# Kernel tuning notes

Hardware: AMD Instinct MI355X
Metric: run time of the kernel (lower is better)

Reference implementation:

```python
import jax, jax.numpy as jnp
import numpy as np

B = 4096          # batch_size * world_size
D = 256           # embedding dim
TEMP = 0.5        # temperature
EPS = 1e-8


def setup_inputs() -> dict:
    key = jax.random.key(0)
    k1, k2 = jax.random.split(key)
    z_i = jax.random.normal(k1, (B, D), dtype=jnp.float32)
    z_j = jax.random.normal(k2, (B, D), dtype=jnp.float32)
    return {"z_i": z_i, "z_j": z_j}


def reference(z_i, z_j):
    N = 2 * B
    z = jnp.concatenate([z_i, z_j], axis=0)                      # [N, D]
    # cosine similarity = normalized dot products (normalize + GEMM)
    norm = jnp.sqrt(jnp.sum(z * z, axis=-1, keepdims=True))
    zn = z / jnp.maximum(norm, EPS)
    sim = (zn @ zn.T) / TEMP                                     # [N, N]
    # positives: pairs (i, i+B) and (i+B, i)
    idx = jnp.arange(N)
    pos = sim[idx, (idx + B) % N]                                # [N]
    # CE with label 0 over [pos, negatives]; the candidate set equals the
    # full sim row minus the diagonal (pos is re-included), so:
    sim_masked = jnp.where(jnp.eye(N, dtype=bool), -jnp.inf, sim)
    lse = jax.nn.logsumexp(sim_masked, axis=1)                   # [N]
    loss = jnp.sum(lse - pos) / N                                # reduction='sum' then /N
    return loss
```

## Files before the change

### kernel.cpp

```cpp
#include <hip/hip_runtime.h>
#include <hip/hip_bf16.h>
#include <cmath>

#define B_SZ 4096
#define N_SZ 8192
#define D_SZ 256
#define EPS 1e-8f
#define EXPC 0.01127105500694503f
#define EXPB -2.8853900817779268f

typedef __attribute__((ext_vector_type(4))) float f32x4;
typedef __attribute__((ext_vector_type(4))) int   i32x4;
typedef __attribute__((ext_vector_type(8))) int   i32x8;


__global__ __launch_bounds__(256) void prep_kernel(const float* __restrict__ zi,
                                                   const float* __restrict__ zj,
                                                   char* __restrict__ znb,
                                                   float* __restrict__ pos) {
    const int wave = threadIdx.x >> 6, lane = threadIdx.x & 63;
    const int i = blockIdx.x * 4 + wave;
    float4 a = reinterpret_cast<const float4*>(zi + (size_t)i * D_SZ)[lane];
    float4 b = reinterpret_cast<const float4*>(zj + (size_t)i * D_SZ)[lane];
    float ssa = a.x * a.x + a.y * a.y + a.z * a.z + a.w * a.w;
    float ssb = b.x * b.x + b.y * b.y + b.z * b.z + b.w * b.w;
    float dab = a.x * b.x + a.y * b.y + a.z * b.z + a.w * b.w;
    #pragma unroll
    for (int off = 32; off; off >>= 1) {
        ssa += __shfl_xor(ssa, off, 64);
        ssb += __shfl_xor(ssb, off, 64);
        dab += __shfl_xor(dab, off, 64);
    }
    const float invna = 1.0f / fmaxf(sqrtf(ssa), EPS);
    const float invnb = 1.0f / fmaxf(sqrtf(ssb), EPS);
    if (lane == 0) {
        float p = dab * invna * invnb * 2.0f;
        pos[i] = p;
        pos[i + B_SZ] = p;
    }
    const float sa = invna * 16.0f, sb = invnb * 16.0f;
    const int koff = (lane >> 2) * 1024 + (lane & 3) * 4;
    {
        int pk = __builtin_amdgcn_cvt_pk_fp8_f32(a.x * sa, a.y * sa, 0, false);
        pk     = __builtin_amdgcn_cvt_pk_fp8_f32(a.z * sa, a.w * sa, pk, true);
        *reinterpret_cast<int*>(znb + (size_t)(i >> 6) * 16384 + koff + (i & 63) * 16) = pk;
    }
    {
        const int r = i + B_SZ;
        int pk = __builtin_amdgcn_cvt_pk_fp8_f32(b.x * sb, b.y * sb, 0, false);
        pk     = __builtin_amdgcn_cvt_pk_fp8_f32(b.z * sb, b.w * sb, pk, true);
        *reinterpret_cast<int*>(znb + (size_t)(r >> 6) * 16384 + koff + (r & 63) * 16) = pk;
    }
}

__global__ __launch_bounds__(256, 2) void simlse_kernel(const char* __restrict__ znb,
                                                        float* __restrict__ partial) {
    const int t = threadIdx.x;
    const int wave = t >> 6, lane = t & 63;

    int bid = blockIdx.x, rt = 0;
    #pragma unroll 1
    for (; rt < 32; ++rt) {
        int cnt = 32 - rt;
        if (bid < cnt) break;
        bid -= cnt;
    }
    const int chunk = rt + bid;
    const bool offdiag = (rt != chunk);
    __shared__ float cs[4][256];

    const int rl = lane & 15;
    const int kg = lane >> 4;
    const int i0 = rt * 256 + wave * 64;

    const char* ap = znb + (size_t)(rt * 4 + wave) * 16384 + rl * 16;
    i32x8 afrag[4][2];
    #pragma unroll
    for (int g = 0; g < 4; ++g)
        #pragma unroll
        for (int kc = 0; kc < 2; ++kc) {
            i32x4 lo = *reinterpret_cast<const i32x4*>(
                ap + (kc * 8 + kg * 2) * 1024 + g * 256);
            i32x4 hi = *reinterpret_cast<const i32x4*>(
                ap + (kc * 8 + kg * 2 + 1) * 1024 + g * 256);
            afrag[g][kc] = __builtin_shufflevector(lo, hi, 0, 1, 2, 3, 4, 5, 6, 7);
        }

    float s_acc[4][4];
    #pragma unroll
    for (int g = 0; g < 4; ++g)
        #pragma unroll
        for (int r = 0; r < 4; ++r) s_acc[g][r] = 0.0f;

    const char* bp0 = znb + (size_t)chunk * 4 * 16384 + kg * 2048 + rl * 16;

    i32x4 nb0 = *reinterpret_cast<const i32x4*>(bp0);
    i32x4 nb1 = *reinterpret_cast<const i32x4*>(bp0 + 1024);
    i32x4 nb2 = *reinterpret_cast<const i32x4*>(bp0 + 8192);
    i32x4 nb3 = *reinterpret_cast<const i32x4*>(bp0 + 9216);

    i32x8 bf0, bf1;
    f32x4 accA[4], accB[4];

    #define PREP_B(F)                                                             \
        {                                                                         \
            bf0 = __builtin_shufflevector(nb0, nb1, 0, 1, 2, 3, 4, 5, 6, 7);      \
            bf1 = __builtin_shufflevector(nb2, nb3, 0, 1, 2, 3, 4, 5, 6, 7);      \
            if ((F) < 15) {                                                       \
                const char* bq = bp0 + (((F) + 1) >> 2) * 16384 +                 \
                                 (((F) + 1) & 3) * 256;                           \
                nb0 = *reinterpret_cast<const i32x4*>(bq);                        \
                nb1 = *reinterpret_cast<const i32x4*>(bq + 1024);                 \
                nb2 = *reinterpret_cast<const i32x4*>(bq + 8192);                 \
                nb3 = *reinterpret_cast<const i32x4*>(bq + 9216);                 \
            }                                                                     \
        }

    #define MFMA8(ACC)                                                            \
        {                                                                         \
            _Pragma("unroll")                                                     \
            for (int g = 0; g < 4; ++g) ACC[g] = (f32x4){0.f, 0.f, 0.f, 0.f};     \
            _Pragma("unroll")                                                     \
            for (int g = 0; g < 4; ++g)                                           \
                asm("v_mfma_f32_16x16x128_f8f6f4 %0, %1, %2, %0"                  \
                    : "+v"(ACC[g]) : "v"(afrag[g][0]), "v"(bf0));                 \
            _Pragma("unroll")                                                     \
            for (int g = 0; g < 4; ++g)                                           \
                asm("v_mfma_f32_16x16x128_f8f6f4 %0, %1, %2, %0"                  \
                    : "+v"(ACC[g]) : "v"(afrag[g][1]), "v"(bf1));                 \
        }

    #define EXPSUM(ACC, F)                                                        \
        {                                                                         \
            float cthr = 0.0f;                                                    \
            _Pragma("unroll")                                                     \
            for (int g = 0; g < 4; ++g)                                           \
                _Pragma("unroll")                                                 \
                for (int r = 0; r < 4; ++r) {                                     \
                    float e = __builtin_amdgcn_exp2f(fmaf(ACC[g][r], EXPC, EXPB)); \
                    s_acc[g][r] += e;                                             \
                    cthr += e;                                                    \
                }                                                                 \
            cthr += __shfl_xor(cthr, 16, 64);                                     \
            cthr += __shfl_xor(cthr, 32, 64);                                     \
            if (offdiag && lane < 16)                                             \
                cs[wave][((F) >> 2) * 64 + ((F) & 3) * 16 + rl] = cthr;           \
        }

    PREP_B(0);
    MFMA8(accA);
    #pragma unroll 1
    for (int fo = 0; fo < 7; ++fo) {
        const int f1 = 2 * fo + 1, f2 = 2 * fo + 2;
        PREP_B(f1); MFMA8(accB);
        asm volatile("s_nop 7");
        EXPSUM(accA, f1 - 1);
        PREP_B(f2); MFMA8(accA);
        asm volatile("s_nop 7");
        EXPSUM(accB, f2 - 1);
    }
    PREP_B(15); MFMA8(accB);
    asm volatile("s_nop 7");
    EXPSUM(accA, 14);
    asm volatile("s_nop 7");
    EXPSUM(accB, 15);

    #pragma unroll
    for (int g = 0; g < 4; ++g)
        #pragma unroll
        for (int r = 0; r < 4; ++r) {
            float v = s_acc[g][r];
            #pragma unroll
            for (int off = 1; off < 16; off <<= 1) v += __shfl_xor(v, off, 64);
            if (rl == 0)
                partial[chunk * N_SZ + i0 + g * 16 + kg * 4 + r] = v;
        }

    if (offdiag) {
        __syncthreads();
        float v = cs[0][t] + cs[1][t] + cs[2][t] + cs[3][t];
        partial[rt * N_SZ + chunk * 256 + t] = v;
    }
    #undef PREP_B
    #undef MFMA8
    #undef EXPSUM
}

__global__ __launch_bounds__(256) void rowsum_kernel(const float* __restrict__ partial,
                                                     const float* __restrict__ pos,
                                                     float* __restrict__ bpart) {
    const int row = blockIdx.x * 256 + threadIdx.x;
    float s = -1.0f;
    #pragma unroll
    for (int c = 0; c < 32; ++c) s += partial[c * N_SZ + row];
    float acc = 2.0f + logf(s) - pos[row];
    #pragma unroll
    for (int off = 32; off; off >>= 1) acc += __shfl_xor(acc, off, 64);
    __shared__ float w[4];
    if ((threadIdx.x & 63) == 0) w[threadIdx.x >> 6] = acc;
    __syncthreads();
    if (threadIdx.x == 0) bpart[blockIdx.x] = w[0] + w[1] + w[2] + w[3];
}

__global__ __launch_bounds__(64) void finsum_kernel(const float* __restrict__ bpart,
                                                    float* __restrict__ out) {
    float v = threadIdx.x < 32 ? bpart[threadIdx.x] : 0.0f;
    #pragma unroll
    for (int off = 32; off; off >>= 1) v += __shfl_xor(v, off, 64);
    if (threadIdx.x == 0) out[0] = v / (float)N_SZ;
}

extern "C" void kernel_launch(void* const* d_in, const int* in_sizes, int n_in,
                              void* d_out, int out_size, void* d_ws, size_t ws_size,
                              hipStream_t stream) {
    const float* zi = (const float*)d_in[0];
    const float* zj = (const float*)d_in[1];

    char* ws = (char*)d_ws;
    char* znb      = ws;
    float* pos     = (float*)(ws + 2097152);
    float* partial = (float*)(ws + 2097152 + 32768);
    float* bpart   = (float*)(ws + 2097152 + 32768 + 1048576);
    float* out = (float*)d_out;

    prep_kernel<<<B_SZ / 4, 256, 0, stream>>>(zi, zj, znb, pos);
    simlse_kernel<<<528, 256, 0, stream>>>(znb, partial);
    rowsum_kernel<<<32, 256, 0, stream>>>(partial, pos, bpart);
    finsum_kernel<<<1, 64, 0, stream>>>(bpart, out);
}
```

Before: 35.12 us.

## Split sim tile columns into 128-wide halves to double block count

Each block of the triangular similarity/LSE kernel now covers a 256-row by 128-column tile instead of 256x256, so the grid grows from 528 to 1056 blocks. Row and column partial sums go to two separate buffers, and rowsum_kernel walks a variable-length range per row tile. The aim is better wave balance and occupancy across the CUs. The cost is more per-block overhead, since A fragments are reloaded twice as often, and a more irregular reduction.

```diff
diff --git a/kernel.cpp b/kernel.cpp
--- a/kernel.cpp
+++ b/kernel.cpp
@@ -54,20 +54,21 @@
 }
 
 __global__ __launch_bounds__(256, 2) void simlse_kernel(const char* __restrict__ znb,
-                                                        float* __restrict__ partial) {
+                                                        float* __restrict__ partial1,
+                                                        float* __restrict__ partial2) {
     const int t = threadIdx.x;
     const int wave = t >> 6, lane = t & 63;
 
     int bid = blockIdx.x, rt = 0;
     #pragma unroll 1
     for (; rt < 32; ++rt) {
-        int cnt = 32 - rt;
+        int cnt = 64 - 2 * rt;
         if (bid < cnt) break;
         bid -= cnt;
     }
-    const int chunk = rt + bid;
-    const bool offdiag = (rt != chunk);
-    __shared__ float cs[4][256];
+    const int c2 = 2 * rt + bid;
+    const bool offdiag = ((c2 >> 1) != rt);
+    __shared__ float cs[4][128];
 
     const int rl = lane & 15;
     const int kg = lane >> 4;
@@ -92,28 +93,28 @@
         #pragma unroll
         for (int r = 0; r < 4; ++r) s_acc[g][r] = 0.0f;
 
-    const char* bp0 = znb + (size_t)chunk * 4 * 16384 + kg * 2048 + rl * 16;
-
-    i32x4 nb0 = *reinterpret_cast<const i32x4*>(bp0);
-    i32x4 nb1 = *reinterpret_cast<const i32x4*>(bp0 + 1024);
-    i32x4 nb2 = *reinterpret_cast<const i32x4*>(bp0 + 8192);
-    i32x4 nb3 = *reinterpret_cast<const i32x4*>(bp0 + 9216);
-
+    const char* bp0 = znb + (size_t)c2 * 2 * 16384 + kg * 2048 + rl * 16;
+
+    i32x4 nbA0, nbA1, nbA2, nbA3;
+    i32x4 nbB0, nbB1, nbB2, nbB3;
     i32x8 bf0, bf1;
     f32x4 accA[4], accB[4];
 
-    #define PREP_B(F)                                                             \
-        {                                                                         \
-            bf0 = __builtin_shufflevector(nb0, nb1, 0, 1, 2, 3, 4, 5, 6, 7);      \
-            bf1 = __builtin_shufflevector(nb2, nb3, 0, 1, 2, 3, 4, 5, 6, 7);      \
-            if ((F) < 15) {                                                       \
-                const char* bq = bp0 + (((F) + 1) >> 2) * 16384 +                 \
-                                 (((F) + 1) & 3) * 256;                           \
-                nb0 = *reinterpret_cast<const i32x4*>(bq);                        \
-                nb1 = *reinterpret_cast<const i32x4*>(bq + 1024);                 \
-                nb2 = *reinterpret_cast<const i32x4*>(bq + 8192);                 \
-                nb3 = *reinterpret_cast<const i32x4*>(bq + 9216);                 \
-            }                                                                     \
+    #define LOAD_A(F)                                                             \
+        {                                                                         \
+            const char* bq = bp0 + ((F) >> 2) * 16384 + ((F) & 3) * 256;          \
+            nbA0 = *reinterpret_cast<const i32x4*>(bq);                           \
+            nbA1 = *reinterpret_cast<const i32x4*>(bq + 1024);                    \
+            nbA2 = *reinterpret_cast<const i32x4*>(bq + 8192);                    \
+            nbA3 = *reinterpret_cast<const i32x4*>(bq + 9216);                    \
+        }
+    #define LOAD_B(F)                                                             \
+        {                                                                         \
+            const char* bq = bp0 + ((F) >> 2) * 16384 + ((F) & 3) * 256;          \
+            nbB0 = *reinterpret_cast<const i32x4*>(bq);                           \
+            nbB1 = *reinterpret_cast<const i32x4*>(bq + 1024);                    \
+            nbB2 = *reinterpret_cast<const i32x4*>(bq + 8192);                    \
+            nbB3 = *reinterpret_cast<const i32x4*>(bq + 9216);                    \
         }
 
     #define MFMA8(ACC)                                                            \
@@ -147,23 +148,35 @@
                 cs[wave][((F) >> 2) * 64 + ((F) & 3) * 16 + rl] = cthr;           \
         }
 
-    PREP_B(0);
+    LOAD_A(0);
+    LOAD_B(1);
+    bf0 = __builtin_shufflevector(nbA0, nbA1, 0, 1, 2, 3, 4, 5, 6, 7);
+    bf1 = __builtin_shufflevector(nbA2, nbA3, 0, 1, 2, 3, 4, 5, 6, 7);
+    LOAD_A(2);
     MFMA8(accA);
     #pragma unroll 1
-    for (int fo = 0; fo < 7; ++fo) {
+    for (int fo = 0; fo < 3; ++fo) {
         const int f1 = 2 * fo + 1, f2 = 2 * fo + 2;
-        PREP_B(f1); MFMA8(accB);
+        bf0 = __builtin_shufflevector(nbB0, nbB1, 0, 1, 2, 3, 4, 5, 6, 7);
+        bf1 = __builtin_shufflevector(nbB2, nbB3, 0, 1, 2, 3, 4, 5, 6, 7);
+        if (f1 + 2 < 8) LOAD_B(f1 + 2);
+        MFMA8(accB);
         asm volatile("s_nop 7");
         EXPSUM(accA, f1 - 1);
-        PREP_B(f2); MFMA8(accA);
+        bf0 = __builtin_shufflevector(nbA0, nbA1, 0, 1, 2, 3, 4, 5, 6, 7);
+        bf1 = __builtin_shufflevector(nbA2, nbA3, 0, 1, 2, 3, 4, 5, 6, 7);
+        if (f2 + 2 < 8) LOAD_A(f2 + 2);
+        MFMA8(accA);
         asm volatile("s_nop 7");
         EXPSUM(accB, f2 - 1);
     }
-    PREP_B(15); MFMA8(accB);
+    bf0 = __builtin_shufflevector(nbB0, nbB1, 0, 1, 2, 3, 4, 5, 6, 7);
+    bf1 = __builtin_shufflevector(nbB2, nbB3, 0, 1, 2, 3, 4, 5, 6, 7);
+    MFMA8(accB);
     asm volatile("s_nop 7");
-    EXPSUM(accA, 14);
+    EXPSUM(accA, 6);
     asm volatile("s_nop 7");
-    EXPSUM(accB, 15);
+    EXPSUM(accB, 7);
 
     #pragma unroll
     for (int g = 0; g < 4; ++g)
@@ -173,26 +186,33 @@
             #pragma unroll
             for (int off = 1; off < 16; off <<= 1) v += __shfl_xor(v, off, 64);
             if (rl == 0)
-                partial[chunk * N_SZ + i0 + g * 16 + kg * 4 + r] = v;
+                partial1[(size_t)c2 * N_SZ + i0 + g * 16 + kg * 4 + r] = v;
         }
 
     if (offdiag) {
         __syncthreads();
-        float v = cs[0][t] + cs[1][t] + cs[2][t] + cs[3][t];
-        partial[rt * N_SZ + chunk * 256 + t] = v;
-    }
-    #undef PREP_B
+        if (t < 128) {
+            float v = cs[0][t] + cs[1][t] + cs[2][t] + cs[3][t];
+            partial2[(size_t)rt * N_SZ + c2 * 128 + t] = v;
+        }
+    }
+    #undef LOAD_A
+    #undef LOAD_B
     #undef MFMA8
     #undef EXPSUM
 }
 
-__global__ __launch_bounds__(256) void rowsum_kernel(const float* __restrict__ partial,
+__global__ __launch_bounds__(256) void rowsum_kernel(const float* __restrict__ partial1,
+                                                     const float* __restrict__ partial2,
                                                      const float* __restrict__ pos,
                                                      float* __restrict__ bpart) {
-    const int row = blockIdx.x * 256 + threadIdx.x;
+    const int T = blockIdx.x;
+    const int row = T * 256 + threadIdx.x;
     float s = -1.0f;
-    #pragma unroll
-    for (int c = 0; c < 32; ++c) s += partial[c * N_SZ + row];
+    #pragma unroll 1
+    for (int c2 = 2 * T; c2 < 64; ++c2) s += partial1[(size_t)c2 * N_SZ + row];
+    #pragma unroll 1
+    for (int r = 0; r < T; ++r) s += partial2[(size_t)r * N_SZ + row];
     float acc = 2.0f + logf(s) - pos[row];
     #pragma unroll
     for (int off = 32; off; off >>= 1) acc += __shfl_xor(acc, off, 64);
@@ -217,14 +237,15 @@
     const float* zj = (const float*)d_in[1];
 
     char* ws = (char*)d_ws;
-    char* znb      = ws;
-    float* pos     = (float*)(ws + 2097152);
-    float* partial = (float*)(ws + 2097152 + 32768);
-    float* bpart   = (float*)(ws + 2097152 + 32768 + 1048576);
+    char* znb       = ws;
+    float* pos      = (float*)(ws + 2097152);
+    float* partial1 = (float*)(ws + 2097152 + 32768);
+    float* partial2 = (float*)(ws + 2097152 + 32768 + 2097152);
+    float* bpart    = (float*)(ws + 2097152 + 32768 + 2097152 + 1048576);
     float* out = (float*)d_out;
 
     prep_kernel<<<B_SZ / 4, 256, 0, stream>>>(zi, zj, znb, pos);
-    simlse_kernel<<<528, 256, 0, stream>>>(znb, partial);
-    rowsum_kernel<<<32, 256, 0, stream>>>(partial, pos, bpart);
+    simlse_kernel<<<1056, 256, 0, stream>>>(znb, partial1, partial2);
+    rowsum_kernel<<<32, 256, 0, stream>>>(partial1, partial2, pos, bpart);
     finsum_kernel<<<1, 64, 0, stream>>>(bpart, out);
 }
```

After: 50.01 us. +42.4%, slower.
